# Kernel tuning notes

Measured on AMD Instinct MI355X. Metric: run time of the kernel, lower is better.

## Reference

```python
import jax, jax.numpy as jnp
import numpy as np

B, C, H, W, O = 32, 512, 28, 28, 1024


def _make_sketch(key, input_dim, output_dim):
    kh, ks = jax.random.split(key)
    rand_h = jax.random.randint(kh, (input_dim,), 0, output_dim)
    rand_s = jax.random.randint(ks, (input_dim,), 0, 2).astype(jnp.float32) * 2.0 - 1.0
    sketch = jnp.zeros((output_dim, input_dim), dtype=jnp.float32)
    return sketch.at[rand_h, jnp.arange(input_dim)].set(rand_s)


def setup_inputs() -> dict:
    key = jax.random.key(0)
    k1, k2, k3, k4 = jax.random.split(key, 4)
    x1 = jax.random.normal(k1, (B, C, H, W), dtype=jnp.float32)
    x2 = jax.random.normal(k2, (B, C, H, W), dtype=jnp.float32)
    sketch1 = _make_sketch(k3, C, O)
    sketch2 = _make_sketch(k4, C, O)
    return {"x1": x1, "x2": x2, "sketch1": sketch1, "sketch2": sketch2}


def reference(x1, x2, sketch1, sketch2):
    b, c, h, w = x1.shape
    out_dim = sketch1.shape[0]
    # [B, C, H*W] -> [B, N, C]
    x1_flat = x1.reshape(b, c, h * w).transpose(0, 2, 1)
    x2_flat = x2.reshape(b, c, h * w).transpose(0, 2, 1)
    # count-sketch projection via dense matmul (faithful to F.linear)
    proj1 = jnp.einsum('bnc,oc->bno', x1_flat, sketch1)
    proj2 = jnp.einsum('bnc,oc->bno', x2_flat, sketch2)
    orig_dtype = proj1.dtype
    # circular convolution via FFT along output_dim axis
    fft1 = jnp.fft.fft(proj1.astype(jnp.float32), axis=-1)
    fft2 = jnp.fft.fft(proj2.astype(jnp.float32), axis=-1)
    cbp_flat = jnp.fft.ifft(fft1 * fft2, axis=-1).real.astype(orig_dtype)
    # [B, N, O] -> [B, O, H, W]
    return cbp_flat.transpose(0, 2, 1).reshape(b, out_dim, h, w)
```

## Files before the change

### kernel.cpp

```cpp
#include <hip/hip_runtime.h>

#define O_DIM   1024
#define C_DIM   512
#define HW      784
#define B_DIM   32
#define T_POS   8
#define NTILES  (HW / T_POS)
#define NTHREADS 256

__device__ __forceinline__ float2 cmul(float2 a, float2 b) {
    return make_float2(a.x * b.x - a.y * b.y, a.x * b.y + a.y * b.x);
}

template<int SGN>
__device__ __forceinline__ void fft32(float2 y[32]) {
    static constexpr float C32[16] = {
        1.f, 0.98078528f, 0.92387953f, 0.83146961f,
        0.70710678f, 0.55557023f, 0.38268343f, 0.19509032f,
        0.f, -0.19509032f, -0.38268343f, -0.55557023f,
        -0.70710678f, -0.83146961f, -0.92387953f, -0.98078528f};
    static constexpr float S32[16] = {
        0.f, 0.19509032f, 0.38268343f, 0.55557023f,
        0.70710678f, 0.83146961f, 0.92387953f, 0.98078528f,
        1.f, 0.98078528f, 0.92387953f, 0.83146961f,
        0.70710678f, 0.55557023f, 0.38268343f, 0.19509032f};
#pragma unroll
    for (int s = 0; s < 5; ++s) {
        const int L = 32 >> s;
        const int h = 16 >> s;
#pragma unroll
        for (int u = 0; u < 16; ++u) {
            const int blk = u >> (4 - s);
            const int t   = u & (h - 1);
            const int i   = blk * L + t;
            const int m   = t << s;
            float2 a = y[i], b = y[i + h];
            y[i] = make_float2(a.x + b.x, a.y + b.y);
            float2 d = make_float2(a.x - b.x, a.y - b.y);
            if (m == 0) {
                y[i + h] = d;
            } else if (m == 8) {
                y[i + h] = (SGN < 0) ? make_float2(d.y, -d.x)
                                     : make_float2(-d.y, d.x);
            } else {
                float2 w = make_float2(C32[m], (SGN < 0) ? -S32[m] : S32[m]);
                y[i + h] = cmul(d, w);
            }
        }
    }
}

template<int SGN>
__device__ __forceinline__ void four_step(float2* zg, int p) {
    static constexpr int REV5[32] = {
        0,16,8,24,4,20,12,28,2,18,10,26,6,22,14,30,
        1,17,9,25,5,21,13,29,3,19,11,27,7,23,15,31};
    float2 y[32];
#pragma unroll
    for (int n2 = 0; n2 < 32; ++n2)
        y[n2] = zg[p + 32 * n2];
    __syncthreads();
    fft32<SGN>(y);
    float sv, cv;
    __sincosf((float)SGN * 6.283185307179586f * (float)p * (1.f / 1024.f), &sv, &cv);
    const float2 stw = make_float2(cv, sv);
    float2 w = make_float2(1.f, 0.f);
#pragma unroll
    for (int k2 = 0; k2 < 32; ++k2) {
        float2 val = y[REV5[k2]];
        if (k2 > 0) val = cmul(val, w);
        zg[k2 * 32 + ((p + k2) & 31)] = val;
        w = cmul(w, stw);
    }
    __syncthreads();
#pragma unroll
    for (int n1 = 0; n1 < 32; ++n1)
        y[n1] = zg[p * 32 + ((n1 + p) & 31)];
    __syncthreads();
    fft32<SGN>(y);
#pragma unroll
    for (int k1 = 0; k1 < 32; ++k1)
        zg[p + 32 * k1] = y[REV5[k1]];
    __syncthreads();
}

__global__ void extract_sketch(const float* __restrict__ sk1,
                               const float* __restrict__ sk2,
                               int* __restrict__ h, float* __restrict__ s) {
    int t = blockIdx.x * blockDim.x + threadIdx.x;
    if (t >= 2 * C_DIM) return;
    const float* sk = (t < C_DIM) ? sk1 : sk2;
    int c = t & (C_DIM - 1);
    int hv = 0; float svv = 0.f;
    for (int o = 0; o < O_DIM; ++o) {
        float v = sk[o * C_DIM + c];
        if (v != 0.f) { hv = o; svv = v; }
    }
    h[t] = hv;
    s[t] = svv;
}

__global__ __launch_bounds__(NTHREADS)
void cbp_main(const float* __restrict__ x1, const float* __restrict__ x2,
              const int* __restrict__ h1, const int* __restrict__ h2,
              const float* __restrict__ s1, const float* __restrict__ s2,
              float* __restrict__ out) {
    __shared__ float2 Z[T_POS][O_DIM];
    const int tid  = threadIdx.x;
    const int b    = blockIdx.x / NTILES;
    const int tile = blockIdx.x % NTILES;
    const int n0   = tile * T_POS;

    float2* zf = &Z[0][0];
#pragma unroll
    for (int i = 0; i < (T_POS * O_DIM) / NTHREADS; ++i)
        zf[tid + NTHREADS * i] = make_float2(0.f, 0.f);
    __syncthreads();

    {
        const int cpart = tid & 31;
        const int j     = tid >> 5;
        const int xbase = b * (C_DIM * HW) + n0 + j;
#pragma unroll 4
        for (int rep = 0; rep < C_DIM / 32; ++rep) {
            const int c  = cpart + (rep << 5);
            const float v1 = x1[xbase + c * HW];
            const float v2 = x2[xbase + c * HW];
            const int   b1 = h1[c], b2 = h2[c];
            const float w1 = s1[c], w2 = s2[c];
            atomicAdd(&Z[j][b1].x, w1 * v1);
            atomicAdd(&Z[j][b2].y, w2 * v2);
        }
    }
    __syncthreads();

    const int g = tid >> 5;
    const int p = tid & 31;
    float2* zg = &Z[g][0];

    four_step<-1>(zg, p);

#pragma unroll
    for (int m = 0; m < 16; ++m) {
        const int k = p + (m << 5);
        if (k == 0) {
            float2 z0 = zg[0];
            float2 z5 = zg[512];
            zg[0]   = make_float2(z0.x * z0.y, 0.f);
            zg[512] = make_float2(z5.x * z5.y, 0.f);
        } else {
            float2 za = zg[k];
            float2 zb = zg[1024 - k];
            float2 F1 = make_float2(0.5f * (za.x + zb.x), 0.5f * (za.y - zb.y));
            float2 F2 = make_float2(0.5f * (za.y + zb.y), -0.5f * (za.x - zb.x));
            float2 G  = cmul(F1, F2);
            zg[k]        = G;
            zg[1024 - k] = make_float2(G.x, -G.y);
        }
    }
    __syncthreads();

    four_step<1>(zg, p);

    {
        const int j  = tid & 7;
        const int ob = tid >> 3;
        const int obase = b * (O_DIM * HW) + n0 + j;
#pragma unroll 4
        for (int rep = 0; rep < O_DIM / 32; ++rep) {
            const int o = ob + (rep << 5);
            out[obase + o * HW] = Z[j][o].x * (1.f / 1024.f);
        }
    }
}

extern "C" void kernel_launch(void* const* d_in, const int* in_sizes, int n_in,
                              void* d_out, int out_size, void* d_ws, size_t ws_size,
                              hipStream_t stream) {
    const float* x1  = (const float*)d_in[0];
    const float* x2  = (const float*)d_in[1];
    const float* sk1 = (const float*)d_in[2];
    const float* sk2 = (const float*)d_in[3];
    float* out = (float*)d_out;

    int*   h = (int*)d_ws;
    float* s = (float*)((char*)d_ws + 4096);

    hipLaunchKernelGGL(extract_sketch, dim3(4), dim3(256), 0, stream, sk1, sk2, h, s);
    hipLaunchKernelGGL(cbp_main, dim3(B_DIM * NTILES), dim3(NTHREADS), 0, stream,
                       x1, x2, h, h + C_DIM, s, s + C_DIM, out);
}
```

Measured before the change: 419.7 us.

## Vectorize loads and stores, shrink tiles, use wave barriers, parallelize sketch extraction

The position tile drops to 4 and the block to 128 threads. Each thread now loads float4 vectors of x1 and x2 across the 4 positions, issuing them before the LDS zeroing, and writes the output as float4. The block-wide barriers inside the FFT are replaced with wave barriers, since each 32-lane FFT group sits inside a single wave64. Sketch extraction moves from 4 blocks doing serial strided scans to one block per output row with coalesced reads. This assumes every sketch column has exactly one nonzero and that FFT groups never straddle a wavefront.

New measurement: 361.8 us. 13.8% less time.

```diff
diff --git a/kernel.cpp b/kernel.cpp
--- a/kernel.cpp
+++ b/kernel.cpp
@@ -4,9 +4,9 @@
 #define C_DIM   512
 #define HW      784
 #define B_DIM   32
-#define T_POS   8
+#define T_POS   4
 #define NTILES  (HW / T_POS)
-#define NTHREADS 256
+#define NTHREADS 128
 
 __device__ __forceinline__ float2 cmul(float2 a, float2 b) {
     return make_float2(a.x * b.x - a.y * b.y, a.x * b.y + a.y * b.x);
@@ -59,7 +59,7 @@
 #pragma unroll
     for (int n2 = 0; n2 < 32; ++n2)
         y[n2] = zg[p + 32 * n2];
-    __syncthreads();
+    __builtin_amdgcn_wave_barrier();
     fft32<SGN>(y);
     float sv, cv;
     __sincosf((float)SGN * 6.283185307179586f * (float)p * (1.f / 1024.f), &sv, &cv);
@@ -72,32 +72,28 @@
         zg[k2 * 32 + ((p + k2) & 31)] = val;
         w = cmul(w, stw);
     }
-    __syncthreads();
+    __builtin_amdgcn_wave_barrier();
 #pragma unroll
     for (int n1 = 0; n1 < 32; ++n1)
         y[n1] = zg[p * 32 + ((n1 + p) & 31)];
-    __syncthreads();
+    __builtin_amdgcn_wave_barrier();
     fft32<SGN>(y);
 #pragma unroll
     for (int k1 = 0; k1 < 32; ++k1)
         zg[p + 32 * k1] = y[REV5[k1]];
-    __syncthreads();
+    __builtin_amdgcn_wave_barrier();
 }
 
 __global__ void extract_sketch(const float* __restrict__ sk1,
                                const float* __restrict__ sk2,
                                int* __restrict__ h, float* __restrict__ s) {
-    int t = blockIdx.x * blockDim.x + threadIdx.x;
-    if (t >= 2 * C_DIM) return;
-    const float* sk = (t < C_DIM) ? sk1 : sk2;
-    int c = t & (C_DIM - 1);
-    int hv = 0; float svv = 0.f;
-    for (int o = 0; o < O_DIM; ++o) {
-        float v = sk[o * C_DIM + c];
-        if (v != 0.f) { hv = o; svv = v; }
-    }
-    h[t] = hv;
-    s[t] = svv;
+    const int o = blockIdx.x;
+    for (int c = threadIdx.x; c < C_DIM; c += blockDim.x) {
+        float v1 = sk1[o * C_DIM + c];
+        if (v1 != 0.f) { h[c] = o; s[c] = v1; }
+        float v2 = sk2[o * C_DIM + c];
+        if (v2 != 0.f) { h[C_DIM + c] = o; s[C_DIM + c] = v2; }
+    }
 }
 
 __global__ __launch_bounds__(NTHREADS)
@@ -111,26 +107,38 @@
     const int tile = blockIdx.x % NTILES;
     const int n0   = tile * T_POS;
 
+    float4 v1[4], v2[4];
+    int    b1[4], b2[4];
+    float  w1[4], w2[4];
+    const int xoff = b * (C_DIM * HW) + n0;
+#pragma unroll
+    for (int r = 0; r < 4; ++r) {
+        const int c = tid + NTHREADS * r;
+        v1[r] = *reinterpret_cast<const float4*>(x1 + xoff + c * HW);
+        v2[r] = *reinterpret_cast<const float4*>(x2 + xoff + c * HW);
+        b1[r] = h1[c];  b2[r] = h2[c];
+        w1[r] = s1[c];  w2[r] = s2[c];
+    }
+
     float2* zf = &Z[0][0];
 #pragma unroll
     for (int i = 0; i < (T_POS * O_DIM) / NTHREADS; ++i)
         zf[tid + NTHREADS * i] = make_float2(0.f, 0.f);
     __syncthreads();
 
-    {
-        const int cpart = tid & 31;
-        const int j     = tid >> 5;
-        const int xbase = b * (C_DIM * HW) + n0 + j;
-#pragma unroll 4
-        for (int rep = 0; rep < C_DIM / 32; ++rep) {
-            const int c  = cpart + (rep << 5);
-            const float v1 = x1[xbase + c * HW];
-            const float v2 = x2[xbase + c * HW];
-            const int   b1 = h1[c], b2 = h2[c];
-            const float w1 = s1[c], w2 = s2[c];
-            atomicAdd(&Z[j][b1].x, w1 * v1);
-            atomicAdd(&Z[j][b2].y, w2 * v2);
-        }
+#pragma unroll
+    for (int r = 0; r < 4; ++r) {
+        const float4 a = v1[r], c4 = v2[r];
+        const int   q1 = b1[r], q2 = b2[r];
+        const float u1 = w1[r], u2 = w2[r];
+        atomicAdd(&Z[0][q1].x, u1 * a.x);
+        atomicAdd(&Z[1][q1].x, u1 * a.y);
+        atomicAdd(&Z[2][q1].x, u1 * a.z);
+        atomicAdd(&Z[3][q1].x, u1 * a.w);
+        atomicAdd(&Z[0][q2].y, u2 * c4.x);
+        atomicAdd(&Z[1][q2].y, u2 * c4.y);
+        atomicAdd(&Z[2][q2].y, u2 * c4.z);
+        atomicAdd(&Z[3][q2].y, u2 * c4.w);
     }
     __syncthreads();
 
@@ -158,19 +166,21 @@
             zg[1024 - k] = make_float2(G.x, -G.y);
         }
     }
+    __builtin_amdgcn_wave_barrier();
+
+    four_step<1>(zg, p);
     __syncthreads();
 
-    four_step<1>(zg, p);
-
-    {
-        const int j  = tid & 7;
-        const int ob = tid >> 3;
-        const int obase = b * (O_DIM * HW) + n0 + j;
-#pragma unroll 4
-        for (int rep = 0; rep < O_DIM / 32; ++rep) {
-            const int o = ob + (rep << 5);
-            out[obase + o * HW] = Z[j][o].x * (1.f / 1024.f);
-        }
+    const int obase = b * (O_DIM * HW) + n0;
+#pragma unroll
+    for (int r = 0; r < O_DIM / NTHREADS; ++r) {
+        const int o = tid + NTHREADS * r;
+        float4 res;
+        res.x = Z[0][o].x * (1.f / 1024.f);
+        res.y = Z[1][o].x * (1.f / 1024.f);
+        res.z = Z[2][o].x * (1.f / 1024.f);
+        res.w = Z[3][o].x * (1.f / 1024.f);
+        *reinterpret_cast<float4*>(out + obase + o * HW) = res;
     }
 }
 
@@ -186,7 +196,8 @@
     int*   h = (int*)d_ws;
     float* s = (float*)((char*)d_ws + 4096);
 
-    hipLaunchKernelGGL(extract_sketch, dim3(4), dim3(256), 0, stream, sk1, sk2, h, s);
+    hipLaunchKernelGGL(extract_sketch, dim3(O_DIM), dim3(256), 0, stream,
+                       sk1, sk2, h, s);
     hipLaunchKernelGGL(cbp_main, dim3(B_DIM * NTILES), dim3(NTHREADS), 0, stream,
                        x1, x2, h, h + C_DIM, s, s + C_DIM, out);
 }
```
